# Kernel optimization log

Hardware: AMD Instinct MI355X
Metric: run time of the kernel (lower is better)

Reference implementation:

```python
import jax, jax.numpy as jnp
import numpy as np

V, E, H, NL, B, T = 32000, 256, 256, 2, 32, 256


def setup_inputs() -> dict:
    key = jax.random.key(0)
    ks = jax.random.split(key, 20)
    s = 0.05
    d = {}
    d['x'] = jax.random.randint(ks[0], (B, T), 0, V)
    d['encoder_output'] = jax.random.normal(ks[1], (T + 1, B, 2 * H), jnp.float32)
    d['encoder_final_state'] = jax.random.normal(ks[2], (2 * NL, B, H), jnp.float32)
    d['embedding'] = jax.random.normal(ks[3], (V, E), jnp.float32) * s
    d['enc_proj_w'] = jax.random.normal(ks[4], (H, 2 * H), jnp.float32) * s
    d['enc_proj_b'] = jnp.zeros((H,), jnp.float32)
    d['attn_wq'] = jax.random.normal(ks[5], (H, H), jnp.float32) * s
    d['attn_wk'] = jax.random.normal(ks[6], (H, H), jnp.float32) * s
    d['attn_wv'] = jax.random.normal(ks[7], (H,), jnp.float32) * s
    d['gru_w_ih0'] = jax.random.normal(ks[8], (3 * H, E + H), jnp.float32) * s
    d['gru_w_hh0'] = jax.random.normal(ks[9], (3 * H, H), jnp.float32) * s
    d['gru_b_ih0'] = jnp.zeros((3 * H,), jnp.float32)
    d['gru_b_hh0'] = jnp.zeros((3 * H,), jnp.float32)
    d['gru_w_ih1'] = jax.random.normal(ks[10], (3 * H, H), jnp.float32) * s
    d['gru_w_hh1'] = jax.random.normal(ks[11], (3 * H, H), jnp.float32) * s
    d['gru_b_ih1'] = jnp.zeros((3 * H,), jnp.float32)
    d['gru_b_hh1'] = jnp.zeros((3 * H,), jnp.float32)
    d['dense_w'] = jax.random.normal(ks[12], (V, H), jnp.float32) * s
    d['dense_b'] = jnp.zeros((V,), jnp.float32)
    return d


def _gru_cell(xin, h, w_ih, w_hh, b_ih, b_hh):
    gi = xin @ w_ih.T + b_ih
    gh = h @ w_hh.T + b_hh
    i_r, i_z, i_n = jnp.split(gi, 3, axis=-1)
    h_r, h_z, h_n = jnp.split(gh, 3, axis=-1)
    r = jax.nn.sigmoid(i_r + h_r)
    z = jax.nn.sigmoid(i_z + h_z)
    n = jnp.tanh(i_n + r * h_n)
    return (1.0 - z) * n + z * h


def _forward(x, encoder_output, encoder_final_state, embedding, enc_proj_w, enc_proj_b,
             attn_wq, attn_wk, attn_wv,
             gru_w_ih0, gru_w_hh0, gru_b_ih0, gru_b_hh0,
             gru_w_ih1, gru_w_hh1, gru_b_ih1, gru_b_hh1,
             dense_w, dense_b):
    Bb, Tt = x.shape
    Hh = enc_proj_w.shape[0]
    L = 2 * Tt  # fixed KV buffer length (= max attention width)
    # project encoder output: (B, T+1, H)
    proj = jnp.einsum('sbd,hd->bsh', encoder_output, enc_proj_w) + enc_proj_b
    # sum forward/backward encoder final states -> (n_layers, B, H)
    h0 = encoder_final_state.reshape(NL, 2, Bb, Hh).sum(axis=1)
    emb = embedding[x].transpose(1, 0, 2)  # (T, B, E)
    # fixed-size KV buffer; slots [0, T+1) hold projected encoder output
    kv0 = jnp.zeros((Bb, L, Hh), proj.dtype).at[:, :Tt + 1, :].set(proj)
    kproj0 = jnp.einsum('blh,gh->blg', kv0, attn_wk)  # precomputed key projections

    def step(carry, inp):
        h, kv, kproj = carry
        emb_t, t = inp
        q = h[-1] @ attn_wq.T  # (B, H)
        scores = jnp.tanh(kproj + q[:, None, :]) @ attn_wv  # (B, L)
        valid = jnp.arange(L) < (Tt + 1 + t)
        attn = jax.nn.softmax(jnp.where(valid[None, :], scores, -1e9), axis=-1)
        attn = attn * valid[None, :].astype(attn.dtype)  # exact zeros at padding
        context = jnp.einsum('bl,blh->bh', attn, kv)
        xin = jnp.concatenate([context, emb_t], axis=-1)  # (B, H+E)
        h0n = _gru_cell(xin, h[0], gru_w_ih0, gru_w_hh0, gru_b_ih0, gru_b_hh0)
        h1n = _gru_cell(h0n, h[1], gru_w_ih1, gru_w_hh1, gru_b_ih1, gru_b_hh1)
        h_new = jnp.stack([h0n, h1n], axis=0)
        out = h1n  # top-layer output for this timestep
        pos = Tt + 1 + t
        kv = jax.lax.dynamic_update_slice_in_dim(kv, out[:, None, :], pos, axis=1)
        kproj = jax.lax.dynamic_update_slice_in_dim(kproj, (out @ attn_wk.T)[:, None, :], pos, axis=1)
        return (h_new, kv, kproj), (out, attn)

    (_, _, _), (outs, attns) = jax.lax.scan(step, (h0, kv0, kproj0), (emb, jnp.arange(Tt)))
    outs = outs.transpose(1, 0, 2)  # (B, T, H)
    logits = jnp.einsum('bth,vh->btv', outs, dense_w) + dense_b  # (B, T, V)
    attn_scores = attns.transpose(1, 0, 2)  # (B, T, 2T)
    return logits, attn_scores


def reference(x, encoder_output, encoder_final_state, embedding, enc_proj_w, enc_proj_b,
              attn_wq, attn_wk, attn_wv,
              gru_w_ih0, gru_w_hh0, gru_b_ih0, gru_b_hh0,
              gru_w_ih1, gru_w_hh1, gru_b_ih1, gru_b_hh1,
              dense_w, dense_b):
    return _forward(x, encoder_output, encoder_final_state, embedding, enc_proj_w, enc_proj_b,
                    attn_wq, attn_wk, attn_wv,
                    gru_w_ih0, gru_w_hh0, gru_b_ih0, gru_b_hh0,
                    gru_w_ih1, gru_w_hh1, gru_b_ih1, gru_b_hh1,
                    dense_w, dense_b)
```

## Files before the change

### kernel.cpp

```cpp
#include <hip/hip_runtime.h>
#include <hip/hip_bf16.h>
#include <hip/hip_fp16.h>

#define NB 32
#define NT 256
#define NH 256
#define NV 32000
#define NL2 512
#define NTP1 257

typedef unsigned int u32x4 __attribute__((ext_vector_type(4)));
typedef unsigned int u32x2 __attribute__((ext_vector_type(2)));
typedef short s16x8 __attribute__((ext_vector_type(8)));
typedef float f32x4 __attribute__((ext_vector_type(4)));
typedef _Float16 half2v __attribute__((ext_vector_type(2)));

#define AGENT __HIP_MEMORY_SCOPE_AGENT
__device__ __forceinline__ float aload(const float* p) {
  return __hip_atomic_load((float*)p, __ATOMIC_RELAXED, AGENT);
}
__device__ __forceinline__ void astore(float* p, float v) {
  __hip_atomic_store(p, v, __ATOMIC_RELAXED, AGENT);
}

__device__ __forceinline__ float dot2f(half2v a, half2v b, float c) {
#if __has_builtin(__builtin_amdgcn_fdot2)
  return __builtin_amdgcn_fdot2(a, b, c, false);
#else
  return c + (float)a[0] * (float)b[0] + (float)a[1] * (float)b[1];
#endif
}
__device__ __forceinline__ half2v h2(unsigned int u) { return __builtin_bit_cast(half2v, u); }

__device__ __forceinline__ float dot16h(const _Float16* __restrict__ w,
                                        const _Float16* __restrict__ x) {
  u32x4 a0 = *(const u32x4*)w;
  u32x4 a1 = *(const u32x4*)(w + 8);
  u32x4 b0 = *(const u32x4*)x;
  u32x4 b1 = *(const u32x4*)(x + 8);
  float acc = 0.f;
  acc = dot2f(h2(a0.x), h2(b0.x), acc);
  acc = dot2f(h2(a0.y), h2(b0.y), acc);
  acc = dot2f(h2(a0.z), h2(b0.z), acc);
  acc = dot2f(h2(a0.w), h2(b0.w), acc);
  acc = dot2f(h2(a1.x), h2(b1.x), acc);
  acc = dot2f(h2(a1.y), h2(b1.y), acc);
  acc = dot2f(h2(a1.z), h2(b1.z), acc);
  acc = dot2f(h2(a1.w), h2(b1.w), acc);
  return acc;
}

__device__ __forceinline__ float fast_tanh(float x) {
  x = fminf(15.f, fmaxf(-15.f, x));
  float e = __expf(2.f * x);
  return 1.f - __fdividef(2.f, e + 1.f);
}
__device__ __forceinline__ float fast_sigmoid(float x) {
  x = fminf(30.f, fmaxf(-30.f, x));
  float e = __expf(-x);
  return __fdividef(1.f, 1.f + e);
}
__device__ __forceinline__ unsigned short f2bf(float f) {
  unsigned int u = __builtin_bit_cast(unsigned int, f);
  return (unsigned short)((u + 0x7FFFu + ((u >> 16) & 1u)) >> 16);
}

__device__ __forceinline__ void batch_barrier(int* __restrict__ ctr, int target) {
  __syncthreads();
  if (threadIdx.x == 0) {
    __hip_atomic_fetch_add(ctr, 1, __ATOMIC_RELEASE, AGENT);
    while (__hip_atomic_load(ctr, __ATOMIC_RELAXED, AGENT) < target)
      __builtin_amdgcn_s_sleep(1);
    asm volatile("" ::: "memory");
  }
  __syncthreads();
}


__global__ void conv_f16_kernel(const float* __restrict__ s, _Float16* __restrict__ d, int n) {
  int i = blockIdx.x * 256 + threadIdx.x;
  if (i < n) d[i] = (_Float16)s[i];
}

__global__ void conv_bf16_kernel(const float* __restrict__ s, unsigned short* __restrict__ d, int n) {
  int i = blockIdx.x * 256 + threadIdx.x;
  if (i < n) d[i] = f2bf(s[i]);
}

__global__ void packT_kernel(const float* __restrict__ w, unsigned int* __restrict__ out,
                             int R, int K) {
  int gid = blockIdx.x * 256 + threadIdx.x;
  int K2 = K >> 1;
  if (gid >= R * K2) return;
  int k2 = gid / R, r = gid - k2 * R;
  unsigned short ua = __builtin_bit_cast(unsigned short, (_Float16)w[(size_t)r * K + 2 * k2]);
  unsigned short ub = __builtin_bit_cast(unsigned short, (_Float16)w[(size_t)r * K + 2 * k2 + 1]);
  out[(size_t)k2 * R + r] = (unsigned int)ua | ((unsigned int)ub << 16);
}

__global__ void transpose_kernel(const float* __restrict__ w, float* __restrict__ wT) {
  int i = blockIdx.x * 256 + threadIdx.x;
  if (i < 256 * 512) { int h = i >> 9, dd = i & 511; wT[dd * 256 + h] = w[i]; }
}

__global__ __launch_bounds__(256) void proj_kernel(const float* __restrict__ enc,
                                                   const float* __restrict__ wT,
                                                   const float* __restrict__ pb,
                                                   _Float16* __restrict__ kvL) {
  int gid = blockIdx.x * 256 + threadIdx.x;
  int h4 = gid & 63;
  int bs = gid >> 6;
  if (bs >= NTP1 * NB) return;
  int s = bs >> 5, b = bs & 31;
  const float* er = enc + (size_t)bs * 512;
  float a0 = 0.f, a1 = 0.f, a2 = 0.f, a3 = 0.f;
  for (int d = 0; d < 512; d += 4) {
    f32x4 e4 = *(const f32x4*)(er + d);
    f32x4 w0 = *(const f32x4*)(wT + (size_t)(d + 0) * 256 + h4 * 4);
    f32x4 w1 = *(const f32x4*)(wT + (size_t)(d + 1) * 256 + h4 * 4);
    f32x4 w2 = *(const f32x4*)(wT + (size_t)(d + 2) * 256 + h4 * 4);
    f32x4 w3 = *(const f32x4*)(wT + (size_t)(d + 3) * 256 + h4 * 4);
    a0 = fmaf(e4.x, w0.x, a0); a1 = fmaf(e4.x, w0.y, a1); a2 = fmaf(e4.x, w0.z, a2); a3 = fmaf(e4.x, w0.w, a3);
    a0 = fmaf(e4.y, w1.x, a0); a1 = fmaf(e4.y, w1.y, a1); a2 = fmaf(e4.y, w1.z, a2); a3 = fmaf(e4.y, w1.w, a3);
    a0 = fmaf(e4.z, w2.x, a0); a1 = fmaf(e4.z, w2.y, a1); a2 = fmaf(e4.z, w2.z, a2); a3 = fmaf(e4.z, w2.w, a3);
    a0 = fmaf(e4.w, w3.x, a0); a1 = fmaf(e4.w, w3.y, a1); a2 = fmaf(e4.w, w3.z, a2); a3 = fmaf(e4.w, w3.w, a3);
  }
  int h = h4 * 4;
  a0 += pb[h + 0]; a1 += pb[h + 1]; a2 += pb[h + 2]; a3 += pb[h + 3];
  _Float16* dst = kvL + ((size_t)b * 512 + s) * 256 + h;
  dst[0] = (_Float16)a0; dst[1] = (_Float16)a1;
  dst[2] = (_Float16)a2; dst[3] = (_Float16)a3;
}

__global__ __launch_bounds__(256) void kproj0_kernel(const _Float16* __restrict__ kvL,
                                                     const float* __restrict__ wk,
                                                     _Float16* __restrict__ kprojL) {
  int b = blockIdx.x >> 3, gq = blockIdx.x & 7;
  __shared__ float wks[32][256];
  __shared__ float pk[32][8];
  int tid = threadIdx.x;
  for (int i = tid; i < 32 * 256; i += 256) {
    int g = i >> 8, h = i & 255;
    wks[g][h] = wk[(size_t)(gq * 32 + g) * 256 + h];
  }
  __syncthreads();
  {
    int l = tid;
    float acc[32];
#pragma unroll
    for (int g = 0; g < 32; ++g) acc[g] = 0.f;
    for (int h = 0; h < 256; ++h) {
      float kvv = (float)kvL[((size_t)b * 512 + l) * 256 + h];
#pragma unroll
      for (int g = 0; g < 32; ++g) acc[g] = fmaf(kvv, wks[g][h], acc[g]);
    }
    for (int g = 0; g < 32; ++g)
      kprojL[((size_t)b * NL2 + l) * NH + gq * 32 + g] = (_Float16)acc[g];
  }
  {
    int g = tid >> 3, hc = tid & 7;
    float acc = 0.f;
    for (int h = hc * 32; h < hc * 32 + 32; ++h)
      acc += (float)kvL[((size_t)b * 512 + 256) * 256 + h] * wks[g][h];
    pk[g][hc] = acc;
    __syncthreads();
    if (tid < 32) {
      float sv = 0.f;
      for (int c = 0; c < 8; ++c) sv += pk[tid][c];
      kprojL[((size_t)b * NL2 + 256) * NH + gq * 32 + tid] = (_Float16)sv;
    }
  }
}


__global__ __launch_bounds__(512) void scan_kernel(
    const int* __restrict__ x, const float* __restrict__ efs, const float* __restrict__ emb,
    const float* __restrict__ wv,
    const float* __restrict__ bih0, const float* __restrict__ bhh0,
    const float* __restrict__ bih1, const float* __restrict__ bhh1,
    const _Float16* __restrict__ wq16, const _Float16* __restrict__ wk16,
    const unsigned int* __restrict__ wih0T, const unsigned int* __restrict__ whh0T,
    const unsigned int* __restrict__ wih1T, const unsigned int* __restrict__ whh1T,
    const unsigned int* __restrict__ kvL_u, const unsigned int* __restrict__ kprojL_u,
    float* __restrict__ spart, float* __restrict__ vec0, float* __restrict__ vec1,
    int* __restrict__ bars,
    unsigned short* __restrict__ outs_bf, float* __restrict__ attn_out) {
  __shared__ __align__(16) unsigned int kp_u[512 * 17];
  __shared__ __align__(16) unsigned int kv_u[512 * 19];
  __shared__ __align__(16) float att[512], gsum[1024];
  __shared__ __align__(16) float h0s[256], h1s[256];
  __shared__ __align__(16) float scr[544], scr2[32 * 35];
  __shared__ __align__(16) float qs[32], wvs[32], red[16];
  __shared__ __align__(16) _Float16 h0h[256], h1h[256], xinh[64];

  int tid = threadIdx.x;
  int b = blockIdx.x & 31;
  int s = blockIdx.x >> 5;
  int* bar = bars + b * 32;

  if (tid < 256) {
    float h0v = efs[(size_t)(0 * NB + b) * NH + tid] + efs[(size_t)(1 * NB + b) * NH + tid];
    float h1v = efs[(size_t)(2 * NB + b) * NH + tid] + efs[(size_t)(3 * NB + b) * NH + tid];
    h0s[tid] = h0v; h0h[tid] = (_Float16)h0v;
    h1s[tid] = h1v; h1h[tid] = (_Float16)h1v;
  }
  if (tid < 32) wvs[tid] = wv[32 * s + tid];
  for (int idx = tid; idx < 257 * 16; idx += 512) {
    int l = idx >> 4, c = idx & 15;
    kp_u[l * 17 + c] = kprojL_u[((size_t)b * 512 + l) * 128 + 16 * s + c];
    kv_u[l * 19 + c] = kvL_u[((size_t)b * 512 + l) * 128 + 16 * s + c];
  }
  for (int idx = tid; idx < 255 * 16; idx += 512) {
    int l = 257 + (idx >> 4), c = idx & 15;
    kp_u[l * 17 + c] = 0u;
    kv_u[l * 19 + c] = 0u;
  }
  __syncthreads();

  for (int t = 0; t < NT; ++t) {
    int Lt = NTP1 + t;
    int tgt = 8 * (t + 1);
    {
      int row = tid & 31, ch = tid >> 5;
      scr[ch * 33 + row] = dot16h(wq16 + (size_t)(32 * s + row) * 256 + ch * 16, h1h + ch * 16);
      if (tid >= 480) {
        int j = tid - 480;
        int tok = x[b * NT + t];
        xinh[32 + j] = (_Float16)emb[(size_t)tok * 256 + 32 * s + j];
      }
    }
    __syncthreads();
    if (tid < 32) {
      float a = 0.f;
#pragma unroll
      for (int c = 0; c < 16; ++c) a += scr[c * 33 + tid];
      qs[tid] = a;
    }
    __syncthreads();
    {
      float acc = 0.f;
      if (tid < Lt) {
        const unsigned int* kr = kp_u + tid * 17;
#pragma unroll 4
        for (int g2 = 0; g2 < 16; ++g2) {
          half2v kp2 = h2(kr[g2]);
          acc = fmaf(wvs[2 * g2 + 0], fast_tanh((float)kp2[0] + qs[2 * g2 + 0]), acc);
          acc = fmaf(wvs[2 * g2 + 1], fast_tanh((float)kp2[1] + qs[2 * g2 + 1]), acc);
        }
      }
      astore(spart + ((size_t)(b * 8 + s)) * 512 + tid, acc);
    }
    batch_barrier(bar + 0, tgt);
    {
      float sum = 0.f;
#pragma unroll
      for (int sp = 0; sp < 8; ++sp) sum += aload(spart + ((size_t)(b * 8 + sp)) * 512 + tid);
      float v = (tid < Lt) ? sum : -3.0e38f;
      float m = v;
#pragma unroll
      for (int off = 32; off; off >>= 1) m = fmaxf(m, __shfl_xor(m, off, 64));
      if ((tid & 63) == 0) red[tid >> 6] = m;
      __syncthreads();
      float M = red[0];
#pragma unroll
      for (int i = 1; i < 8; ++i) M = fmaxf(M, red[i]);
      float e = (tid < Lt) ? __expf(v - M) : 0.f;
      float zz = e;
#pragma unroll
      for (int off = 32; off; off >>= 1) zz += __shfl_xor(zz, off, 64);
      if ((tid & 63) == 0) red[8 + (tid >> 6)] = zz;
      __syncthreads();
      float Z = red[8];
#pragma unroll
      for (int i = 1; i < 8; ++i) Z += red[8 + i];
      float a = __fdividef(e, Z);
      att[tid] = a;
      if ((tid >> 6) == s) attn_out[((size_t)(b * NT + t)) * NL2 + tid] = a;
    }
    __syncthreads();
    {
      int c = tid >> 4, hh = tid & 15;
      float aA = 0.f, aB = 0.f;
#pragma unroll
      for (int j = 0; j < 16; ++j) {
        int l = 16 * c + j;
        half2v kv2 = h2(kv_u[l * 19 + hh]);
        float av = att[l];
        aA = fmaf((float)kv2[0], av, aA);
        aB = fmaf((float)kv2[1], av, aB);
      }
      scr2[c * 35 + 2 * hh] = aA;
      scr2[c * 35 + 2 * hh + 1] = aB;
    }
    __syncthreads();
    if (tid < 32) {
      float a = 0.f;
#pragma unroll
      for (int c = 0; c < 32; ++c) a += scr2[c * 35 + tid];
      xinh[tid] = (_Float16)a;
    }
    __syncthreads();
    {
      const unsigned int* xu = (const unsigned int*)xinh;
      const unsigned int* h0u = (const unsigned int*)h0h;
      float accA = 0.f, accI = 0.f, accH = 0.f;
      bool dual = (tid < 256);
#pragma unroll 2
      for (int i = 0; i < 16; ++i) {
        unsigned int xc = xu[i], xe = xu[16 + i];
        const unsigned int* wc = wih0T + (size_t)(16 * s + i) * 768;
        const unsigned int* we = wih0T + (size_t)(128 + 16 * s + i) * 768;
        accA = dot2f(h2(wc[tid]), h2(xc), accA);
        accA = dot2f(h2(we[tid]), h2(xe), accA);
        if (dual) {
          accI = dot2f(h2(wc[512 + tid]), h2(xc), accI);
          accI = dot2f(h2(we[512 + tid]), h2(xe), accI);
        }
      }
#pragma unroll 2
      for (int i = 0; i < 16; ++i) {
        unsigned int hv = h0u[16 * s + i];
        const unsigned int* wr = whh0T + (size_t)(16 * s + i) * 768;
        accA = dot2f(h2(wr[tid]), h2(hv), accA);
        if (dual) accH = dot2f(h2(wr[512 + tid]), h2(hv), accH);
      }
      float* vb = vec0 + (size_t)(b * 8 + s) * 1024;
      astore(vb + tid, accA);
      if (dual) { astore(vb + 512 + tid, accI); astore(vb + 768 + tid, accH); }
    }
    batch_barrier(bar + 1, tgt);
    {
      float t0 = 0.f, t1 = 0.f;
#pragma unroll
      for (int sp = 0; sp < 8; ++sp) {
        const float* vb = vec0 + (size_t)(b * 8 + sp) * 1024;
        t0 += aload(vb + tid);
        t1 += aload(vb + 512 + tid);
      }
      gsum[tid] = t0; gsum[512 + tid] = t1;
    }
    __syncthreads();
    if (tid < 256) {
      float rr = fast_sigmoid(gsum[tid] + bih0[tid] + bhh0[tid]);
      float zz = fast_sigmoid(gsum[256 + tid] + bih0[256 + tid] + bhh0[256 + tid]);
      float nn = fast_tanh(gsum[512 + tid] + bih0[512 + tid] + rr * (gsum[768 + tid] + bhh0[512 + tid]));
      float hv = (1.f - zz) * nn + zz * h0s[tid];
      h0s[tid] = hv; h0h[tid] = (_Float16)hv;
    }
    __syncthreads();
    {
      const unsigned int* h0u = (const unsigned int*)h0h;
      const unsigned int* h1u = (const unsigned int*)h1h;
      float accA = 0.f, accI = 0.f, accH = 0.f;
      bool dual = (tid < 256);
#pragma unroll 2
      for (int i = 0; i < 16; ++i) {
        unsigned int xv = h0u[16 * s + i];
        unsigned int hv = h1u[16 * s + i];
        const unsigned int* wi = wih1T + (size_t)(16 * s + i) * 768;
        const unsigned int* wh = whh1T + (size_t)(16 * s + i) * 768;
        accA = dot2f(h2(wi[tid]), h2(xv), accA);
        accA = dot2f(h2(wh[tid]), h2(hv), accA);
        if (dual) {
          accI = dot2f(h2(wi[512 + tid]), h2(xv), accI);
          accH = dot2f(h2(wh[512 + tid]), h2(hv), accH);
        }
      }
      float* vb = vec1 + (size_t)(b * 8 + s) * 1024;
      astore(vb + tid, accA);
      if (dual) { astore(vb + 512 + tid, accI); astore(vb + 768 + tid, accH); }
    }
    batch_barrier(bar + 2, tgt);
    {
      float t0 = 0.f, t1 = 0.f;
#pragma unroll
      for (int sp = 0; sp < 8; ++sp) {
        const float* vb = vec1 + (size_t)(b * 8 + sp) * 1024;
        t0 += aload(vb + tid);
        t1 += aload(vb + 512 + tid);
      }
      gsum[tid] = t0; gsum[512 + tid] = t1;
    }
    __syncthreads();
    if (tid < 256) {
      float rr = fast_sigmoid(gsum[tid] + bih1[tid] + bhh1[tid]);
      float zz = fast_sigmoid(gsum[256 + tid] + bih1[256 + tid] + bhh1[256 + tid]);
      float nn = fast_tanh(gsum[512 + tid] + bih1[512 + tid] + rr * (gsum[768 + tid] + bhh1[512 + tid]));
      float hv = (1.f - zz) * nn + zz * h1s[tid];
      h1s[tid] = hv; h1h[tid] = (_Float16)hv;
      if ((tid >> 5) == s) outs_bf[((size_t)(b * NT + t)) * NH + tid] = f2bf(hv);
    }
    __syncthreads();
    if (t < NT - 1) {
      int pos = NTP1 + t;
      if (tid < 16) {
        unsigned short lo = __builtin_bit_cast(unsigned short, h1h[32 * s + 2 * tid]);
        unsigned short hi = __builtin_bit_cast(unsigned short, h1h[32 * s + 2 * tid + 1]);
        kv_u[pos * 19 + tid] = (unsigned int)lo | ((unsigned int)hi << 16);
      }
      {
        int row = tid & 31, ch = tid >> 5;
        scr[ch * 33 + row] = dot16h(wk16 + (size_t)(32 * s + row) * 256 + ch * 16, h1h + ch * 16);
      }
      __syncthreads();
      if (tid < 32) {
        float a = 0.f;
#pragma unroll
        for (int c = 0; c < 16; ++c) a += scr[c * 33 + tid];
        ((_Float16*)kp_u)[pos * 34 + tid] = (_Float16)a;
      }
      __syncthreads();
    }
  }
}


__global__ __launch_bounds__(256) void logits_gemm(const unsigned short* __restrict__ A,
                                                   const unsigned short* __restrict__ Bw,
                                                   const float* __restrict__ bias,
                                                   float* __restrict__ C) {
  __shared__ unsigned short As[128][88];
  __shared__ unsigned short Bs[128][88];
  int tid = threadIdx.x;
  int nt = blockIdx.x % 250, mt = blockIdx.x / 250;
  int m0 = mt * 128, n0 = nt * 128;
  int lane = tid & 63, w = tid >> 6;
  int wm = w & 1, wn = w >> 1;
  f32x4 acc[4][4];
#pragma unroll
  for (int m = 0; m < 4; ++m)
#pragma unroll
    for (int n = 0; n < 4; ++n) acc[m][n] = (f32x4)0.0f;

  int r0 = tid >> 3;
  int c0 = (tid & 7) * 8;
  for (int kt = 0; kt < 4; ++kt) {
    __syncthreads();
#pragma unroll
    for (int it = 0; it < 4; ++it) {
      int row = it * 32 + r0;
      u32x4 va = *(const u32x4*)(A + (size_t)(m0 + row) * 256 + kt * 64 + c0);
      u32x4 vb = *(const u32x4*)(Bw + (size_t)(n0 + row) * 256 + kt * 64 + c0);
      *(u32x4*)(&As[row][c0]) = va;
      *(u32x4*)(&Bs[row][c0]) = vb;
    }
    __syncthreads();
#pragma unroll
    for (int ks = 0; ks < 2; ++ks) {
      s16x8 af[4], bf[4];
#pragma unroll
      for (int m = 0; m < 4; ++m)
        af[m] = *(const s16x8*)(&As[wm * 64 + m * 16 + (lane & 15)][ks * 32 + (lane >> 4) * 8]);
#pragma unroll
      for (int n = 0; n < 4; ++n)
        bf[n] = *(const s16x8*)(&Bs[wn * 64 + n * 16 + (lane & 15)][ks * 32 + (lane >> 4) * 8]);
#pragma unroll
      for (int m = 0; m < 4; ++m)
#pragma unroll
        for (int n = 0; n < 4; ++n)
          acc[m][n] = __builtin_amdgcn_mfma_f32_16x16x32_bf16(af[m], bf[n], acc[m][n], 0, 0, 0);
    }
  }
#pragma unroll
  for (int n = 0; n < 4; ++n) {
    int col = n0 + wn * 64 + n * 16 + (lane & 15);
    float bv = bias[col];
#pragma unroll
    for (int m = 0; m < 4; ++m) {
      int rowb = m0 + wm * 64 + m * 16 + (lane >> 4) * 4;
#pragma unroll
      for (int r = 0; r < 4; ++r)
        C[(size_t)(rowb + r) * NV + col] = acc[m][n][r] + bv;
    }
  }
}


extern "C" void kernel_launch(void* const* d_in, const int* in_sizes, int n_in,
                              void* d_out, int out_size, void* d_ws, size_t ws_size,
                              hipStream_t stream) {
  const int*   x    = (const int*)d_in[0];
  const float* enc  = (const float*)d_in[1];
  const float* efs  = (const float*)d_in[2];
  const float* emb  = (const float*)d_in[3];
  const float* epw  = (const float*)d_in[4];
  const float* epb  = (const float*)d_in[5];
  const float* wq   = (const float*)d_in[6];
  const float* wk   = (const float*)d_in[7];
  const float* wv   = (const float*)d_in[8];
  const float* wih0 = (const float*)d_in[9];
  const float* whh0 = (const float*)d_in[10];
  const float* bih0 = (const float*)d_in[11];
  const float* bhh0 = (const float*)d_in[12];
  const float* wih1 = (const float*)d_in[13];
  const float* whh1 = (const float*)d_in[14];
  const float* bih1 = (const float*)d_in[15];
  const float* bhh1 = (const float*)d_in[16];
  const float* dw   = (const float*)d_in[17];
  const float* db   = (const float*)d_in[18];

  const size_t o_alias  = 0;
  const size_t a_wq16   = 0;
  const size_t a_wk16   = a_wq16 + 131072;
  const size_t a_wih0T  = a_wk16 + 131072;
  const size_t a_whh0T  = a_wih0T + 786432;
  const size_t a_wih1T  = a_whh0T + 393216;
  const size_t a_whh1T  = a_wih1T + 393216;
  const size_t a_kvL    = a_whh1T + 393216;
  const size_t o_wT     = o_alias + 16384000;
  const size_t o_kprojL = o_wT + 524288;
  const size_t o_outs   = o_kprojL + 8388608;
  const size_t o_spart  = o_outs + 4194304;
  const size_t o_vec0   = o_spart + 524288;
  const size_t o_vec1   = o_vec0 + 1048576;
  const size_t o_bar    = o_vec1 + 1048576;
  const size_t need     = o_bar + 4096;
  if (ws_size < need) return;

  char* ws = (char*)d_ws;
  unsigned short* dwbf16 = (unsigned short*)(ws + o_alias);
  _Float16* wq16     = (_Float16*)(ws + a_wq16);
  _Float16* wk16     = (_Float16*)(ws + a_wk16);
  unsigned int* wih0T = (unsigned int*)(ws + a_wih0T);
  unsigned int* whh0T = (unsigned int*)(ws + a_whh0T);
  unsigned int* wih1T = (unsigned int*)(ws + a_wih1T);
  unsigned int* whh1T = (unsigned int*)(ws + a_whh1T);
  _Float16* kvL      = (_Float16*)(ws + a_kvL);
  float* wT          = (float*)(ws + o_wT);
  _Float16* kprojL   = (_Float16*)(ws + o_kprojL);
  unsigned short* outs_bf = (unsigned short*)(ws + o_outs);
  float* spart       = (float*)(ws + o_spart);
  float* vec0        = (float*)(ws + o_vec0);
  float* vec1        = (float*)(ws + o_vec1);
  int* bars          = (int*)(ws + o_bar);

  float* logits = (float*)d_out;
  float* attn_out = logits + (size_t)NB * NT * NV;

  hipMemsetAsync(ws + o_bar, 0, 4096, stream);

  conv_f16_kernel<<<(65536 + 255) / 256, 256, 0, stream>>>(wq, wq16, 65536);
  conv_f16_kernel<<<(65536 + 255) / 256, 256, 0, stream>>>(wk, wk16, 65536);
  packT_kernel<<<(768 * 256 + 255) / 256, 256, 0, stream>>>(wih0, wih0T, 768, 512);
  packT_kernel<<<(768 * 128 + 255) / 256, 256, 0, stream>>>(whh0, whh0T, 768, 256);
  packT_kernel<<<(768 * 128 + 255) / 256, 256, 0, stream>>>(wih1, wih1T, 768, 256);
  packT_kernel<<<(768 * 128 + 255) / 256, 256, 0, stream>>>(whh1, whh1T, 768, 256);
  transpose_kernel<<<(131072 + 255) / 256, 256, 0, stream>>>(epw, wT);

  proj_kernel<<<(NTP1 * NB * 64) / 256, 256, 0, stream>>>(enc, wT, epb, kvL);
  kproj0_kernel<<<NB * 8, 256, 0, stream>>>(kvL, wk, kprojL);

  scan_kernel<<<256, 512, 0, stream>>>(x, efs, emb, wv, bih0, bhh0, bih1, bhh1,
                                       wq16, wk16, wih0T, whh0T, wih1T, whh1T,
                                       (const unsigned int*)kvL, (const unsigned int*)kprojL,
                                       spart, vec0, vec1, bars,
                                       outs_bf, attn_out);

  conv_bf16_kernel<<<(8192000 + 255) / 256, 256, 0, stream>>>(dw, dwbf16, 8192000);

  logits_gemm<<<(NB * NT / 128) * (NV / 128), 256, 0, stream>>>(outs_bf, dwbf16, db, logits);
}
```

Before: 7.129 ms.

## Repartition scan across blocks by sequence position to cut inter-block barriers

The per-batch scan is restructured so each of the 8 cooperating blocks owns 64 key/value positions (full hidden width) instead of a 32-wide slice of the hidden dimension. Attention is computed locally with a per-block max and sum that are merged via an online-softmax rescale. The context GEMV, layer-0 input and hidden GEMVs are fused into one exchange, and layer 1 is computed per block on its own hidden slice. This cuts the global barriers per timestep from three to about two, and the q/k projections are computed as partial sums for the next step. The cost is more partial-sum traffic through global memory, a more complex rescaled reduction, and different precision and layout paths for several weights.

After: 20.83 ms. 192% more time.

```diff
diff --git a/kernel.cpp b/kernel.cpp
--- a/kernel.cpp
+++ b/kernel.cpp
@@ -10,7 +10,6 @@
 #define NTP1 257
 
 typedef unsigned int u32x4 __attribute__((ext_vector_type(4)));
-typedef unsigned int u32x2 __attribute__((ext_vector_type(2)));
 typedef short s16x8 __attribute__((ext_vector_type(8)));
 typedef float f32x4 __attribute__((ext_vector_type(4)));
 typedef _Float16 half2v __attribute__((ext_vector_type(2)));
@@ -65,7 +64,7 @@
   return (unsigned short)((u + 0x7FFFu + ((u >> 16) & 1u)) >> 16);
 }
 
-__device__ __forceinline__ void batch_barrier(int* __restrict__ ctr, int target) {
+__device__ __forceinline__ void bar_step(int* __restrict__ ctr, int target) {
   __syncthreads();
   if (threadIdx.x == 0) {
     __hip_atomic_fetch_add(ctr, 1, __ATOMIC_RELEASE, AGENT);
@@ -178,238 +177,293 @@
     const float* __restrict__ wv,
     const float* __restrict__ bih0, const float* __restrict__ bhh0,
     const float* __restrict__ bih1, const float* __restrict__ bhh1,
-    const _Float16* __restrict__ wq16, const _Float16* __restrict__ wk16,
+    const unsigned int* __restrict__ wqT, const unsigned int* __restrict__ wkT,
     const unsigned int* __restrict__ wih0T, const unsigned int* __restrict__ whh0T,
-    const unsigned int* __restrict__ wih1T, const unsigned int* __restrict__ whh1T,
+    const _Float16* __restrict__ wih1f, const _Float16* __restrict__ whh1f,
     const unsigned int* __restrict__ kvL_u, const unsigned int* __restrict__ kprojL_u,
-    float* __restrict__ spart, float* __restrict__ vec0, float* __restrict__ vec1,
+    float* __restrict__ b1buf, float* __restrict__ b2buf,
     int* __restrict__ bars,
     unsigned short* __restrict__ outs_bf, float* __restrict__ attn_out) {
-  __shared__ __align__(16) unsigned int kp_u[512 * 17];
-  __shared__ __align__(16) unsigned int kv_u[512 * 19];
-  __shared__ __align__(16) float att[512], gsum[1024];
-  __shared__ __align__(16) float h0s[256], h1s[256];
-  __shared__ __align__(16) float scr[544], scr2[32 * 35];
-  __shared__ __align__(16) float qs[32], wvs[32], red[16];
-  __shared__ __align__(16) _Float16 h0h[256], h1h[256], xinh[64];
+  __shared__ __align__(16) _Float16 kv16[64 * 258];
+  __shared__ __align__(16) _Float16 kp16[64 * 258];
+  __shared__ __align__(16) _Float16 h0h[256], h1h[256], h1q[32];
+  __shared__ __align__(16) float q_f[256], wvf[256], h0f[256], h1f[256];
+  __shared__ __align__(16) float ctmp[2][256], ctxf[256], score_e[64], scr9[64 * 9];
+  __shared__ __align__(16) float gi0f[768], gh0f[768], sgi[96], sgh[96];
+  __shared__ __align__(16) float msz[2], mzv[16];
+  __shared__ __align__(16) unsigned int ctxp_u[128], embp_u[16];
 
   int tid = threadIdx.x;
   int b = blockIdx.x & 31;
   int s = blockIdx.x >> 5;
-  int* bar = bars + b * 32;
+  int* barB1 = bars + b * 32 + 0;
+  int* barB2 = bars + b * 32 + 1;
+  float* b2w = b2buf + ((size_t)(b * 8 + s)) * 2368;
+  float* b1w = b1buf + ((size_t)(b * 8 + s)) * 576;
 
   if (tid < 256) {
     float h0v = efs[(size_t)(0 * NB + b) * NH + tid] + efs[(size_t)(1 * NB + b) * NH + tid];
     float h1v = efs[(size_t)(2 * NB + b) * NH + tid] + efs[(size_t)(3 * NB + b) * NH + tid];
-    h0s[tid] = h0v; h0h[tid] = (_Float16)h0v;
-    h1s[tid] = h1v; h1h[tid] = (_Float16)h1v;
-  }
-  if (tid < 32) wvs[tid] = wv[32 * s + tid];
-  for (int idx = tid; idx < 257 * 16; idx += 512) {
-    int l = idx >> 4, c = idx & 15;
-    kp_u[l * 17 + c] = kprojL_u[((size_t)b * 512 + l) * 128 + 16 * s + c];
-    kv_u[l * 19 + c] = kvL_u[((size_t)b * 512 + l) * 128 + 16 * s + c];
-  }
-  for (int idx = tid; idx < 255 * 16; idx += 512) {
-    int l = 257 + (idx >> 4), c = idx & 15;
-    kp_u[l * 17 + c] = 0u;
-    kv_u[l * 19 + c] = 0u;
+    h0f[tid] = h0v; h0h[tid] = (_Float16)h0v;
+    h1f[tid] = h1v; h1h[tid] = (_Float16)h1v;
+    wvf[tid] = wv[tid];
+  }
+  for (int idx = tid; idx < 64 * 128; idx += 512) {
+    int lr = idx >> 7, c = idx & 127;
+    int l = 64 * s + lr;
+    unsigned int kpv = 0u, kvv = 0u;
+    if (l < NTP1) {
+      kpv = kprojL_u[((size_t)b * 512 + l) * 128 + c];
+      kvv = kvL_u[((size_t)b * 512 + l) * 128 + c];
+    }
+    ((unsigned int*)kp16)[lr * 129 + c] = kpv;
+    ((unsigned int*)kv16)[lr * 129 + c] = kvv;
   }
   __syncthreads();
+  if (tid < 32) h1q[tid] = h1h[32 * s + tid];
+  __syncthreads();
+  if (tid < 256) {
+    float a = 0.f;
+#pragma unroll
+    for (int i = 0; i < 16; ++i)
+      a = dot2f(h2(wqT[(size_t)(16 * s + i) * 256 + tid]), h2(((const unsigned int*)h1q)[i]), a);
+    astore(b1w + tid, a);
+    if (tid < 16)
+      astore(b1w + 512 + tid, __builtin_bit_cast(float, ((const unsigned int*)h1q)[tid]));
+  }
+  bar_step(barB1, 0);
 
   for (int t = 0; t < NT; ++t) {
     int Lt = NTP1 + t;
     int tgt = 8 * (t + 1);
+    if (tid == 0) {
+      while (__hip_atomic_load(barB1, __ATOMIC_RELAXED, AGENT) < tgt)
+        __builtin_amdgcn_s_sleep(1);
+      asm volatile("" ::: "memory");
+    }
+    __syncthreads();
+    if (tid < 256) {
+      float a = 0.f;
+#pragma unroll
+      for (int sp = 0; sp < 8; ++sp) a += aload(b1buf + ((size_t)(b * 8 + sp)) * 576 + tid);
+      q_f[tid] = a;
+    } else if (tid < 384) {
+      int k = tid - 256;
+      int sp = k >> 4, i = k & 15;
+      unsigned int u = __builtin_bit_cast(unsigned int,
+          aload(b1buf + ((size_t)(b * 8 + sp)) * 576 + 512 + i));
+      half2v p = h2(u);
+      h1h[32 * sp + 2 * i] = p[0]; h1h[32 * sp + 2 * i + 1] = p[1];
+      h1f[32 * sp + 2 * i] = (float)p[0]; h1f[32 * sp + 2 * i + 1] = (float)p[1];
+    }
+    __syncthreads();
+    if (t >= 1) {
+      int l_app = 256 + t;
+      if ((l_app >> 6) == s) {
+        int lr = l_app - 64 * s;
+        if (tid < 256) {
+          float a = 0.f;
+#pragma unroll
+          for (int sp = 0; sp < 8; ++sp)
+            a += aload(b1buf + ((size_t)(b * 8 + sp)) * 576 + 256 + tid);
+          kp16[lr * 258 + tid] = (_Float16)a;
+        } else {
+          int h = tid - 256;
+          kv16[lr * 258 + h] = h1h[h];
+        }
+      }
+    }
+    __syncthreads();
     {
-      int row = tid & 31, ch = tid >> 5;
-      scr[ch * 33 + row] = dot16h(wq16 + (size_t)(32 * s + row) * 256 + ch * 16, h1h + ch * 16);
-      if (tid >= 480) {
-        int j = tid - 480;
-        int tok = x[b * NT + t];
-        xinh[32 + j] = (_Float16)emb[(size_t)tok * 256 + 32 * s + j];
-      }
+      int lr = tid >> 3, gc = tid & 7;
+      const unsigned int* kpr = (const unsigned int*)kp16 + lr * 129 + gc * 16;
+      const float* qg = q_f + gc * 32;
+      const float* wg = wvf + gc * 32;
+      float part = 0.f;
+#pragma unroll
+      for (int j = 0; j < 16; ++j) {
+        half2v kp2 = h2(kpr[j]);
+        part = fmaf(wg[2 * j], fast_tanh((float)kp2[0] + qg[2 * j]), part);
+        part = fmaf(wg[2 * j + 1], fast_tanh((float)kp2[1] + qg[2 * j + 1]), part);
+      }
+      scr9[lr * 9 + gc] = part;
+    }
+    __syncthreads();
+    if (tid < 64) {
+      int l = 64 * s + tid;
+      float sc = 0.f;
+#pragma unroll
+      for (int c = 0; c < 8; ++c) sc += scr9[tid * 9 + c];
+      sc = (l < Lt) ? sc : -3.0e38f;
+      float m = sc;
+#pragma unroll
+      for (int off = 32; off; off >>= 1) m = fmaxf(m, __shfl_xor(m, off, 64));
+      float e = __expf(sc - m);
+      score_e[tid] = e;
+      float z = e;
+#pragma unroll
+      for (int off = 32; off; off >>= 1) z += __shfl_xor(z, off, 64);
+      if (tid == 0) { msz[0] = m; msz[1] = z; }
+    }
+    __syncthreads();
+    {
+      int h = tid & 255, half = tid >> 8;
+      const _Float16* kvb = kv16 + half * 32 * 258 + h;
+      const float* ep = score_e + half * 32;
+      float c = 0.f;
+#pragma unroll 8
+      for (int j = 0; j < 32; ++j) c = fmaf(ep[j], (float)kvb[j * 258], c);
+      ctmp[half][h] = c;
+    }
+    __syncthreads();
+    if (tid < 256) ctxf[tid] = ctmp[0][tid] + ctmp[1][tid];
+    __syncthreads();
+    if (tid < 128) {
+      unsigned short lo = __builtin_bit_cast(unsigned short, (_Float16)ctxf[2 * tid]);
+      unsigned short hi = __builtin_bit_cast(unsigned short, (_Float16)ctxf[2 * tid + 1]);
+      ctxp_u[tid] = (unsigned int)lo | ((unsigned int)hi << 16);
+    } else if (tid < 144) {
+      int i = tid - 128;
+      int tok = x[b * NT + t];
+      unsigned short lo = __builtin_bit_cast(unsigned short, (_Float16)emb[(size_t)tok * 256 + 32 * s + 2 * i]);
+      unsigned short hi = __builtin_bit_cast(unsigned short, (_Float16)emb[(size_t)tok * 256 + 32 * s + 2 * i + 1]);
+      embp_u[i] = (unsigned int)lo | ((unsigned int)hi << 16);
+    }
+    __syncthreads();
+    {
+      bool dual = (tid < 256);
+      float y1 = 0.f, y2 = 0.f;
+      const unsigned int* wp = wih0T + tid;
+#pragma unroll 8
+      for (int k2 = 0; k2 < 128; ++k2) {
+        unsigned int cp = ctxp_u[k2];
+        y1 = dot2f(h2(wp[(size_t)k2 * 768]), h2(cp), y1);
+        if (dual) y2 = dot2f(h2(wp[(size_t)k2 * 768 + 512]), h2(cp), y2);
+      }
+      astore(b2w + tid, y1);
+      if (dual) astore(b2w + 512 + tid, y2);
+      float ui1 = 0.f, ui2 = 0.f, uh1 = 0.f, uh2 = 0.f;
+      const unsigned int* h0p = (const unsigned int*)h0h;
+#pragma unroll
+      for (int i = 0; i < 16; ++i) {
+        unsigned int ep = embp_u[i];
+        unsigned int hp = h0p[16 * s + i];
+        const unsigned int* we = wih0T + (size_t)(128 + 16 * s + i) * 768;
+        const unsigned int* wh = whh0T + (size_t)(16 * s + i) * 768;
+        ui1 = dot2f(h2(we[tid]), h2(ep), ui1);
+        uh1 = dot2f(h2(wh[tid]), h2(hp), uh1);
+        if (dual) {
+          ui2 = dot2f(h2(we[512 + tid]), h2(ep), ui2);
+          uh2 = dot2f(h2(wh[512 + tid]), h2(hp), uh2);
+        }
+      }
+      astore(b2w + 768 + tid, ui1);
+      astore(b2w + 1536 + tid, uh1);
+      if (dual) {
+        astore(b2w + 768 + 512 + tid, ui2);
+        astore(b2w + 1536 + 512 + tid, uh2);
+      }
+      if (tid == 0) { astore(b2w + 2304, msz[0]); astore(b2w + 2305, msz[1]); }
+    }
+    bar_step(barB2, tgt);
+    if (tid < 8) {
+      const float* p = b2buf + ((size_t)(b * 8 + tid)) * 2368;
+      mzv[2 * tid] = aload(p + 2304);
+      mzv[2 * tid + 1] = aload(p + 2305);
+    }
+    __syncthreads();
+    float M = mzv[0];
+#pragma unroll
+    for (int i = 1; i < 8; ++i) M = fmaxf(M, mzv[2 * i]);
+    float alph[8];
+    float Zg = 0.f;
+#pragma unroll
+    for (int sp = 0; sp < 8; ++sp) {
+      alph[sp] = __expf(mzv[2 * sp] - M);
+      Zg = fmaf(alph[sp], mzv[2 * sp + 1], Zg);
+    }
+    float rZ = __fdividef(1.f, Zg);
+    {
+      bool dual = (tid < 256);
+      float gy1 = 0.f, gu1 = 0.f, gv1 = 0.f, gy2 = 0.f, gu2 = 0.f, gv2 = 0.f;
+#pragma unroll
+      for (int sp = 0; sp < 8; ++sp) {
+        const float* p = b2buf + ((size_t)(b * 8 + sp)) * 2368;
+        gy1 = fmaf(alph[sp], aload(p + tid), gy1);
+        gu1 += aload(p + 768 + tid);
+        gv1 += aload(p + 1536 + tid);
+        if (dual) {
+          gy2 = fmaf(alph[sp], aload(p + 512 + tid), gy2);
+          gu2 += aload(p + 768 + 512 + tid);
+          gv2 += aload(p + 1536 + 512 + tid);
+        }
+      }
+      gi0f[tid] = gy1 * rZ + gu1 + bih0[tid];
+      gh0f[tid] = gv1 + bhh0[tid];
+      if (dual) {
+        gi0f[512 + tid] = gy2 * rZ + gu2 + bih0[512 + tid];
+        gh0f[512 + tid] = gv2 + bhh0[512 + tid];
+      }
+    }
+    __syncthreads();
+    if (tid < 256) {
+      float r_ = fast_sigmoid(gi0f[tid] + gh0f[tid]);
+      float z_ = fast_sigmoid(gi0f[256 + tid] + gh0f[256 + tid]);
+      float n_ = fast_tanh(gi0f[512 + tid] + r_ * gh0f[512 + tid]);
+      float hv = (1.f - z_) * n_ + z_ * h0f[tid];
+      h0f[tid] = hv; h0h[tid] = (_Float16)hv;
+    } else if (tid < 320) {
+      int j = tid - 256;
+      attn_out[((size_t)(b * NT + t)) * NL2 + 64 * s + j] = score_e[j] * alph[s] * rZ;
+    }
+    __syncthreads();
+    if (tid < 384) {
+      int rr = tid >> 2, sub = tid & 3;
+      int g_ = rr >> 5, j = rr & 31;
+      int grow = g_ * 256 + 32 * s + j;
+      const _Float16* wi = wih1f + (size_t)grow * 256 + sub * 64;
+      const _Float16* wh = whh1f + (size_t)grow * 256 + sub * 64;
+      float gi = 0.f, gh = 0.f;
+#pragma unroll
+      for (int i = 0; i < 4; ++i) {
+        gi += dot16h(wi + i * 16, h0h + sub * 64 + i * 16);
+        gh += dot16h(wh + i * 16, h1h + sub * 64 + i * 16);
+      }
+      gi += __shfl_xor(gi, 1); gi += __shfl_xor(gi, 2);
+      gh += __shfl_xor(gh, 1); gh += __shfl_xor(gh, 2);
+      if (sub == 0) { sgi[rr] = gi; sgh[rr] = gh; }
     }
     __syncthreads();
     if (tid < 32) {
-      float a = 0.f;
-#pragma unroll
-      for (int c = 0; c < 16; ++c) a += scr[c * 33 + tid];
-      qs[tid] = a;
-    }
-    __syncthreads();
-    {
-      float acc = 0.f;
-      if (tid < Lt) {
-        const unsigned int* kr = kp_u + tid * 17;
-#pragma unroll 4
-        for (int g2 = 0; g2 < 16; ++g2) {
-          half2v kp2 = h2(kr[g2]);
-          acc = fmaf(wvs[2 * g2 + 0], fast_tanh((float)kp2[0] + qs[2 * g2 + 0]), acc);
-          acc = fmaf(wvs[2 * g2 + 1], fast_tanh((float)kp2[1] + qs[2 * g2 + 1]), acc);
-        }
-      }
-      astore(spart + ((size_t)(b * 8 + s)) * 512 + tid, acc);
-    }
-    batch_barrier(bar + 0, tgt);
-    {
-      float sum = 0.f;
-#pragma unroll
-      for (int sp = 0; sp < 8; ++sp) sum += aload(spart + ((size_t)(b * 8 + sp)) * 512 + tid);
-      float v = (tid < Lt) ? sum : -3.0e38f;
-      float m = v;
-#pragma unroll
-      for (int off = 32; off; off >>= 1) m = fmaxf(m, __shfl_xor(m, off, 64));
-      if ((tid & 63) == 0) red[tid >> 6] = m;
+      int j = tid, hj = 32 * s + j;
+      float r_ = fast_sigmoid(sgi[j] + bih1[hj] + sgh[j] + bhh1[hj]);
+      float z_ = fast_sigmoid(sgi[32 + j] + bih1[256 + hj] + sgh[32 + j] + bhh1[256 + hj]);
+      float n_ = fast_tanh(sgi[64 + j] + bih1[512 + hj] + r_ * (sgh[64 + j] + bhh1[512 + hj]));
+      float hv = (1.f - z_) * n_ + z_ * h1f[hj];
+      outs_bf[((size_t)(b * NT + t)) * NH + hj] = f2bf(hv);
+      h1q[j] = (_Float16)hv;
+    }
+    __syncthreads();
+    if (t < NT - 1) {
+      if (tid < 256) {
+        float a = 0.f;
+#pragma unroll
+        for (int i = 0; i < 16; ++i)
+          a = dot2f(h2(wqT[(size_t)(16 * s + i) * 256 + tid]), h2(((const unsigned int*)h1q)[i]), a);
+        astore(b1w + tid, a);
+        if (tid < 16)
+          astore(b1w + 512 + tid, __builtin_bit_cast(float, ((const unsigned int*)h1q)[tid]));
+      } else {
+        int g = tid - 256;
+        float a = 0.f;
+#pragma unroll
+        for (int i = 0; i < 16; ++i)
+          a = dot2f(h2(wkT[(size_t)(16 * s + i) * 256 + g]), h2(((const unsigned int*)h1q)[i]), a);
+        astore(b1w + 256 + g, a);
+      }
       __syncthreads();
-      float M = red[0];
-#pragma unroll
-      for (int i = 1; i < 8; ++i) M = fmaxf(M, red[i]);
-      float e = (tid < Lt) ? __expf(v - M) : 0.f;
-      float zz = e;
-#pragma unroll
-      for (int off = 32; off; off >>= 1) zz += __shfl_xor(zz, off, 64);
-      if ((tid & 63) == 0) red[8 + (tid >> 6)] = zz;
-      __syncthreads();
-      float Z = red[8];
-#pragma unroll
-      for (int i = 1; i < 8; ++i) Z += red[8 + i];
-      float a = __fdividef(e, Z);
-      att[tid] = a;
-      if ((tid >> 6) == s) attn_out[((size_t)(b * NT + t)) * NL2 + tid] = a;
-    }
-    __syncthreads();
-    {
-      int c = tid >> 4, hh = tid & 15;
-      float aA = 0.f, aB = 0.f;
-#pragma unroll
-      for (int j = 0; j < 16; ++j) {
-        int l = 16 * c + j;
-        half2v kv2 = h2(kv_u[l * 19 + hh]);
-        float av = att[l];
-        aA = fmaf((float)kv2[0], av, aA);
-        aB = fmaf((float)kv2[1], av, aB);
-      }
-      scr2[c * 35 + 2 * hh] = aA;
-      scr2[c * 35 + 2 * hh + 1] = aB;
-    }
-    __syncthreads();
-    if (tid < 32) {
-      float a = 0.f;
-#pragma unroll
-      for (int c = 0; c < 32; ++c) a += scr2[c * 35 + tid];
-      xinh[tid] = (_Float16)a;
-    }
-    __syncthreads();
-    {
-      const unsigned int* xu = (const unsigned int*)xinh;
-      const unsigned int* h0u = (const unsigned int*)h0h;
-      float accA = 0.f, accI = 0.f, accH = 0.f;
-      bool dual = (tid < 256);
-#pragma unroll 2
-      for (int i = 0; i < 16; ++i) {
-        unsigned int xc = xu[i], xe = xu[16 + i];
-        const unsigned int* wc = wih0T + (size_t)(16 * s + i) * 768;
-        const unsigned int* we = wih0T + (size_t)(128 + 16 * s + i) * 768;
-        accA = dot2f(h2(wc[tid]), h2(xc), accA);
-        accA = dot2f(h2(we[tid]), h2(xe), accA);
-        if (dual) {
-          accI = dot2f(h2(wc[512 + tid]), h2(xc), accI);
-          accI = dot2f(h2(we[512 + tid]), h2(xe), accI);
-        }
-      }
-#pragma unroll 2
-      for (int i = 0; i < 16; ++i) {
-        unsigned int hv = h0u[16 * s + i];
-        const unsigned int* wr = whh0T + (size_t)(16 * s + i) * 768;
-        accA = dot2f(h2(wr[tid]), h2(hv), accA);
-        if (dual) accH = dot2f(h2(wr[512 + tid]), h2(hv), accH);
-      }
-      float* vb = vec0 + (size_t)(b * 8 + s) * 1024;
-      astore(vb + tid, accA);
-      if (dual) { astore(vb + 512 + tid, accI); astore(vb + 768 + tid, accH); }
-    }
-    batch_barrier(bar + 1, tgt);
-    {
-      float t0 = 0.f, t1 = 0.f;
-#pragma unroll
-      for (int sp = 0; sp < 8; ++sp) {
-        const float* vb = vec0 + (size_t)(b * 8 + sp) * 1024;
-        t0 += aload(vb + tid);
-        t1 += aload(vb + 512 + tid);
-      }
-      gsum[tid] = t0; gsum[512 + tid] = t1;
-    }
-    __syncthreads();
-    if (tid < 256) {
-      float rr = fast_sigmoid(gsum[tid] + bih0[tid] + bhh0[tid]);
-      float zz = fast_sigmoid(gsum[256 + tid] + bih0[256 + tid] + bhh0[256 + tid]);
-      float nn = fast_tanh(gsum[512 + tid] + bih0[512 + tid] + rr * (gsum[768 + tid] + bhh0[512 + tid]));
-      float hv = (1.f - zz) * nn + zz * h0s[tid];
-      h0s[tid] = hv; h0h[tid] = (_Float16)hv;
-    }
-    __syncthreads();
-    {
-      const unsigned int* h0u = (const unsigned int*)h0h;
-      const unsigned int* h1u = (const unsigned int*)h1h;
-      float accA = 0.f, accI = 0.f, accH = 0.f;
-      bool dual = (tid < 256);
-#pragma unroll 2
-      for (int i = 0; i < 16; ++i) {
-        unsigned int xv = h0u[16 * s + i];
-        unsigned int hv = h1u[16 * s + i];
-        const unsigned int* wi = wih1T + (size_t)(16 * s + i) * 768;
-        const unsigned int* wh = whh1T + (size_t)(16 * s + i) * 768;
-        accA = dot2f(h2(wi[tid]), h2(xv), accA);
-        accA = dot2f(h2(wh[tid]), h2(hv), accA);
-        if (dual) {
-          accI = dot2f(h2(wi[512 + tid]), h2(xv), accI);
-          accH = dot2f(h2(wh[512 + tid]), h2(hv), accH);
-        }
-      }
-      float* vb = vec1 + (size_t)(b * 8 + s) * 1024;
-      astore(vb + tid, accA);
-      if (dual) { astore(vb + 512 + tid, accI); astore(vb + 768 + tid, accH); }
-    }
-    batch_barrier(bar + 2, tgt);
-    {
-      float t0 = 0.f, t1 = 0.f;
-#pragma unroll
-      for (int sp = 0; sp < 8; ++sp) {
-        const float* vb = vec1 + (size_t)(b * 8 + sp) * 1024;
-        t0 += aload(vb + tid);
-        t1 += aload(vb + 512 + tid);
-      }
-      gsum[tid] = t0; gsum[512 + tid] = t1;
-    }
-    __syncthreads();
-    if (tid < 256) {
-      float rr = fast_sigmoid(gsum[tid] + bih1[tid] + bhh1[tid]);
-      float zz = fast_sigmoid(gsum[256 + tid] + bih1[256 + tid] + bhh1[256 + tid]);
-      float nn = fast_tanh(gsum[512 + tid] + bih1[512 + tid] + rr * (gsum[768 + tid] + bhh1[512 + tid]));
-      float hv = (1.f - zz) * nn + zz * h1s[tid];
-      h1s[tid] = hv; h1h[tid] = (_Float16)hv;
-      if ((tid >> 5) == s) outs_bf[((size_t)(b * NT + t)) * NH + tid] = f2bf(hv);
-    }
-    __syncthreads();
-    if (t < NT - 1) {
-      int pos = NTP1 + t;
-      if (tid < 16) {
-        unsigned short lo = __builtin_bit_cast(unsigned short, h1h[32 * s + 2 * tid]);
-        unsigned short hi = __builtin_bit_cast(unsigned short, h1h[32 * s + 2 * tid + 1]);
-        kv_u[pos * 19 + tid] = (unsigned int)lo | ((unsigned int)hi << 16);
-      }
-      {
-        int row = tid & 31, ch = tid >> 5;
-        scr[ch * 33 + row] = dot16h(wk16 + (size_t)(32 * s + row) * 256 + ch * 16, h1h + ch * 16);
-      }
-      __syncthreads();
-      if (tid < 32) {
-        float a = 0.f;
-#pragma unroll
-        for (int c = 0; c < 16; ++c) a += scr[c * 33 + tid];
-        ((_Float16*)kp_u)[pos * 34 + tid] = (_Float16)a;
-      }
-      __syncthreads();
+      if (tid == 0)
+        __hip_atomic_fetch_add(barB1, 1, __ATOMIC_RELEASE, AGENT);
     }
   }
 }
@@ -500,60 +554,58 @@
   const float* db   = (const float*)d_in[18];
 
   const size_t o_alias  = 0;
-  const size_t a_wq16   = 0;
-  const size_t a_wk16   = a_wq16 + 131072;
-  const size_t a_wih0T  = a_wk16 + 131072;
+  const size_t a_wqT    = 0;
+  const size_t a_wkT    = a_wqT + 131072;
+  const size_t a_wih0T  = a_wkT + 131072;
   const size_t a_whh0T  = a_wih0T + 786432;
-  const size_t a_wih1T  = a_whh0T + 393216;
-  const size_t a_whh1T  = a_wih1T + 393216;
-  const size_t a_kvL    = a_whh1T + 393216;
+  const size_t a_wih1f  = a_whh0T + 393216;
+  const size_t a_whh1f  = a_wih1f + 393216;
+  const size_t a_kvL    = a_whh1f + 393216;
   const size_t o_wT     = o_alias + 16384000;
   const size_t o_kprojL = o_wT + 524288;
   const size_t o_outs   = o_kprojL + 8388608;
-  const size_t o_spart  = o_outs + 4194304;
-  const size_t o_vec0   = o_spart + 524288;
-  const size_t o_vec1   = o_vec0 + 1048576;
-  const size_t o_bar    = o_vec1 + 1048576;
+  const size_t o_b1     = o_outs + 4194304;
+  const size_t o_b2     = o_b1 + 589824;
+  const size_t o_bar    = o_b2 + 2424832;
   const size_t need     = o_bar + 4096;
   if (ws_size < need) return;
 
   char* ws = (char*)d_ws;
   unsigned short* dwbf16 = (unsigned short*)(ws + o_alias);
-  _Float16* wq16     = (_Float16*)(ws + a_wq16);
-  _Float16* wk16     = (_Float16*)(ws + a_wk16);
+  unsigned int* wqT   = (unsigned int*)(ws + a_wqT);
+  unsigned int* wkT   = (unsigned int*)(ws + a_wkT);
   unsigned int* wih0T = (unsigned int*)(ws + a_wih0T);
   unsigned int* whh0T = (unsigned int*)(ws + a_whh0T);
-  unsigned int* wih1T = (unsigned int*)(ws + a_wih1T);
-  unsigned int* whh1T = (unsigned int*)(ws + a_whh1T);
-  _Float16* kvL      = (_Float16*)(ws + a_kvL);
-  float* wT          = (float*)(ws + o_wT);
-  _Float16* kprojL   = (_Float16*)(ws + o_kprojL);
+  _Float16* wih1f     = (_Float16*)(ws + a_wih1f);
+  _Float16* whh1f     = (_Float16*)(ws + a_whh1f);
+  _Float16* kvL       = (_Float16*)(ws + a_kvL);
+  float* wT           = (float*)(ws + o_wT);
+  _Float16* kprojL    = (_Float16*)(ws + o_kprojL);
   unsigned short* outs_bf = (unsigned short*)(ws + o_outs);
-  float* spart       = (float*)(ws + o_spart);
-  float* vec0        = (float*)(ws + o_vec0);
-  float* vec1        = (float*)(ws + o_vec1);
-  int* bars          = (int*)(ws + o_bar);
+  float* b1buf        = (float*)(ws + o_b1);
+  float* b2buf        = (float*)(ws + o_b2);
+  int* bars           = (int*)(ws + o_bar);
 
   float* logits = (float*)d_out;
   float* attn_out = logits + (size_t)NB * NT * NV;
 
   hipMemsetAsync(ws + o_bar, 0, 4096, stream);
 
-  conv_f16_kernel<<<(65536 + 255) / 256, 256, 0, stream>>>(wq, wq16, 65536);
-  conv_f16_kernel<<<(65536 + 255) / 256, 256, 0, stream>>>(wk, wk16, 65536);
+  packT_kernel<<<(256 * 128 + 255) / 256, 256, 0, stream>>>(wq, wqT, 256, 256);
+  packT_kernel<<<(256 * 128 + 255) / 256, 256, 0, stream>>>(wk, wkT, 256, 256);
   packT_kernel<<<(768 * 256 + 255) / 256, 256, 0, stream>>>(wih0, wih0T, 768, 512);
   packT_kernel<<<(768 * 128 + 255) / 256, 256, 0, stream>>>(whh0, whh0T, 768, 256);
-  packT_kernel<<<(768 * 128 + 255) / 256, 256, 0, stream>>>(wih1, wih1T, 768, 256);
-  packT_kernel<<<(768 * 128 + 255) / 256, 256, 0, stream>>>(whh1, whh1T, 768, 256);
+  conv_f16_kernel<<<(196608 + 255) / 256, 256, 0, stream>>>(wih1, wih1f, 196608);
+  conv_f16_kernel<<<(196608 + 255) / 256, 256, 0, stream>>>(whh1, whh1f, 196608);
   transpose_kernel<<<(131072 + 255) / 256, 256, 0, stream>>>(epw, wT);
 
   proj_kernel<<<(NTP1 * NB * 64) / 256, 256, 0, stream>>>(enc, wT, epb, kvL);
   kproj0_kernel<<<NB * 8, 256, 0, stream>>>(kvL, wk, kprojL);
 
   scan_kernel<<<256, 512, 0, stream>>>(x, efs, emb, wv, bih0, bhh0, bih1, bhh1,
-                                       wq16, wk16, wih0T, whh0T, wih1T, whh1T,
+                                       wqT, wkT, wih0T, whh0T, wih1f, whh1f,
                                        (const unsigned int*)kvL, (const unsigned int*)kprojL,
-                                       spart, vec0, vec1, bars,
+                                       b1buf, b2buf, bars,
                                        outs_bf, attn_out);
 
   conv_bf16_kernel<<<(8192000 + 255) / 256, 256, 0, stream>>>(dw, dwbf16, 8192000);
```
